# Kernel tuning notes

Measured on AMD Instinct MI355X. Metric: run time of the kernel, lower is better.

The kernel has to match this reference:

```python
import jax, jax.numpy as jnp
import numpy as np

T = 4096   # reference sequence length (concatenated virtual samples)
L = 4096   # modality sequence length
D_Q = 64   # reference feature dim
D_QK = 128 # projected query/key dim (before add_one -> 129)
D_V = 128  # value dim
N_IDS = 8  # number of virtual samples encoded in idx


def setup_inputs() -> dict:
    key = jax.random.key(0)
    ks = jax.random.split(key, 20)
    inp = {}
    inp['ref_data'] = jax.random.normal(ks[0], (1, 1, T, D_Q), jnp.float32)
    inp['ref_time'] = jnp.sort(jax.random.uniform(ks[1], (1, T), jnp.float32), axis=-1)
    inp['ref_idx'] = jnp.sort(jax.random.randint(ks[2], (T,), 0, N_IDS))
    inp['m1_data'] = jax.random.normal(ks[3], (1, 1, L, 130), jnp.float32)
    inp['m1_time'] = jnp.sort(jax.random.uniform(ks[4], (1, L), jnp.float32), axis=-1)
    inp['m1_idx'] = jnp.sort(jax.random.randint(ks[5], (L,), 0, N_IDS))
    inp['m2_data'] = jax.random.normal(ks[6], (1, 1, L, 66), jnp.float32)
    inp['m2_time'] = jnp.sort(jax.random.uniform(ks[7], (1, L), jnp.float32), axis=-1)
    inp['m2_idx'] = jnp.sort(jax.random.randint(ks[8], (L,), 0, N_IDS))
    s = 0.05
    inp['Wq'] = jax.random.normal(ks[9], (D_Q, D_QK), jnp.float32) * s
    inp['bq'] = jnp.zeros((D_QK,), jnp.float32)
    inp['Wk1'] = jax.random.normal(ks[10], (1, D_QK), jnp.float32) * s
    inp['bk1'] = jnp.zeros((D_QK,), jnp.float32)
    inp['Wv1'] = jax.random.normal(ks[11], (128, D_V), jnp.float32) * s
    inp['bv1'] = jnp.zeros((D_V,), jnp.float32)
    inp['Wk2'] = jax.random.normal(ks[12], (1, D_QK), jnp.float32) * s
    inp['bk2'] = jnp.zeros((D_QK,), jnp.float32)
    inp['Wv2'] = jax.random.normal(ks[13], (64, D_V), jnp.float32) * s
    inp['bv2'] = jnp.zeros((D_V,), jnp.float32)
    inp['log_tau1'] = jnp.zeros((), jnp.float32)  # log(init_tau=1)
    inp['log_tau2'] = jnp.zeros((), jnp.float32)
    return inp


def _add_one_q(x):  # add_one(x, dim=1): append ones on last axis
    return jnp.concatenate([x, jnp.ones(x.shape[:-1] + (1,), x.dtype)], axis=-1)


def _feat_k(x):  # add_one(x, dim=0): [ones, -x]
    return jnp.concatenate([jnp.ones(x.shape[:-1] + (1,), x.dtype), -x], axis=-1)


def _uni_attn(Q, mdata, q_t, kv_t, q_idx, kv_idx, Wk, bk, Wv, bv, log_tau):
    # qk_type='time': keys from last feature (timestamp), values from data[..., :-2]
    K = _feat_k(mdata[..., -1:] @ Wk + bk)          # (1,1,L,d_qk+1)
    V = mdata[..., :-2] @ Wv + bv                   # (1,1,L,d_v)
    tau = jnp.exp(log_tau)
    # gaussian weight: -(Q.K)^2 / tau
    A = -jnp.square(jnp.einsum('nhtc,nhlc->nhtl', Q, K)) / tau  # (1,1,T,L)
    causal = (q_t[:, :, None] >= kv_t[:, None, :]).astype(Q.dtype)[:, None]  # (1,1,T,L)
    neg_inf = jnp.array(-jnp.inf, Q.dtype)
    bm = jnp.where(q_idx[None, :, None] == kv_idx[None, None, :], jnp.zeros((), Q.dtype), neg_inf)  # (1,T,L)
    fully_masked = jnp.all(jnp.isneginf(bm), axis=-1, keepdims=True)
    safe = jnp.where(fully_masked, jnp.zeros((), Q.dtype), bm)[:, None]  # (1,1,T,L)
    A = jax.nn.softmax(A * causal + safe, axis=-1) * causal
    return jnp.einsum('nhtl,nhlc->nhtc', A, V)      # (1,1,T,d_v)


def reference(ref_data, ref_time, m1_data, m1_time, m2_data, m2_time,
              Wq, bq, Wk1, bk1, Wv1, bv1, Wk2, bk2, Wv2, bv2,
              log_tau1, log_tau2, ref_idx, m1_idx, m2_idx):
    Q = _add_one_q(ref_data @ Wq + bq)  # (1,1,T,d_qk+1)
    y1 = _uni_attn(Q, m1_data, ref_time, m1_time, ref_idx, m1_idx, Wk1, bk1, Wv1, bv1, log_tau1)
    y2 = _uni_attn(Q, m2_data, ref_time, m2_time, ref_idx, m2_idx, Wk2, bk2, Wv2, bv2, log_tau2)
    return jnp.concatenate([y1, y2], axis=-1)  # (1,1,T,2*d_v)
```

## Files before the change

kernel.cpp:

```cpp
#include <hip/hip_runtime.h>
#include <hip/hip_bf16.h>

#define TQ 4096
#define LK 4096
#define QT 16
#define NSPLIT 4
#define CHJ 32

template<bool BF> __device__ __forceinline__ float ld(const void* p, int i);
template<> __device__ __forceinline__ float ld<true>(const void* p, int i) {
    return __bfloat162float(((const __hip_bfloat16*)p)[i]);
}
template<> __device__ __forceinline__ float ld<false>(const void* p, int i) {
    return ((const float*)p)[i];
}
template<bool BF> __device__ __forceinline__ float2 ld2(const void* p, int i);
template<> __device__ __forceinline__ float2 ld2<false>(const void* p, int i) {
    return *(const float2*)((const float*)p + i);
}
template<> __device__ __forceinline__ float2 ld2<true>(const void* p, int i) {
    float2 r; r.x = ld<true>(p, i); r.y = ld<true>(p, i + 1); return r;
}
template<bool BF> __device__ __forceinline__ float4 ld4(const void* p, int i);
template<> __device__ __forceinline__ float4 ld4<false>(const void* p, int i) {
    return *(const float4*)((const float*)p + i);
}
template<> __device__ __forceinline__ float4 ld4<true>(const void* p, int i) {
    float4 r; r.x = ld<true>(p, i); r.y = ld<true>(p, i + 1);
    r.z = ld<true>(p, i + 2); r.w = ld<true>(p, i + 3); return r;
}
template<bool BF> __device__ __forceinline__ void st4(void* p, int i, float4 v);
template<> __device__ __forceinline__ void st4<true>(void* p, int i, float4 v) {
    __hip_bfloat16* o = (__hip_bfloat16*)p + i;
    o[0] = __float2bfloat16(v.x); o[1] = __float2bfloat16(v.y);
    o[2] = __float2bfloat16(v.z); o[3] = __float2bfloat16(v.w);
}
template<> __device__ __forceinline__ void st4<false>(void* p, int i, float4 v) {
    *(float4*)((float*)p + i) = v;
}

__device__ __forceinline__ bool sniff_bf16(const void* ref_time) {
    const int lane = threadIdx.x & 63;
    bool ok = true;
    if (lane < 32) {
        float v = __bfloat162float(((const __hip_bfloat16*)ref_time)[2 * lane]);
        ok = (v >= 0.0f) && (v <= 1.0f);
    }
    return __ballot(ok) == ~0ULL;
}

template<bool BF>
__device__ int ub_time(const void* arr, int n, float key) {
    int lo = 0, hi = n;
    while (lo < hi) { int mid = (lo + hi) >> 1; if (ld<BF>(arr, mid) <= key) lo = mid + 1; else hi = mid; }
    return lo;
}
__device__ int lb_int(const int* arr, int n, int key) {
    int lo = 0, hi = n;
    while (lo < hi) { int mid = (lo + hi) >> 1; if (arr[mid] < key) lo = mid + 1; else hi = mid; }
    return lo;
}
__device__ int ub_int(const int* arr, int n, int key) {
    int lo = 0, hi = n;
    while (lo < hi) { int mid = (lo + hi) >> 1; if (arr[mid] <= key) lo = mid + 1; else hi = mid; }
    return lo;
}

template<bool BF>
__device__ void prep_body(
    const void* ref_data, const void* ref_time, const int* ref_idx,
    const void* m1_time, const int* m1_idx, const void* m2_time, const int* m2_idx,
    const void* Wq, const void* bq,
    const void* Wk1, const void* bk1, const void* Wk2, const void* bk2,
    float* alpha1, float* beta1, float* alpha2, float* beta2,
    int* c1, int* s1, int* e1, int* c2, int* s2, int* e2)
{
    const int lane = threadIdx.x;
    const int t0 = blockIdx.x * 4;

    float rq[4];
    #pragma unroll
    for (int k = 0; k < 4; ++k) rq[k] = ld<BF>(ref_data, (t0 + k) * 64 + lane);

    const float bq0 = ld<BF>(bq, lane), bq1 = ld<BF>(bq, 64 + lane);
    float a0[4], a1[4];
    #pragma unroll
    for (int k = 0; k < 4; ++k) { a0[k] = bq0; a1[k] = bq1; }

    #pragma unroll 16
    for (int i = 0; i < 64; ++i) {
        const float w0 = ld<BF>(Wq, i * 128 + lane);
        const float w1 = ld<BF>(Wq, i * 128 + 64 + lane);
        #pragma unroll
        for (int k = 0; k < 4; ++k) {
            const float x = __shfl(rq[k], i);
            a0[k] = fmaf(x, w0, a0[k]);
            a1[k] = fmaf(x, w1, a1[k]);
        }
    }

    const float wk1lo = (lane >= 1) ? ld<BF>(Wk1, lane - 1) : 0.0f;
    const float wk1hi = ld<BF>(Wk1, lane + 63);
    const float bk1lo = (lane >= 1) ? ld<BF>(bk1, lane - 1) : 0.0f;
    const float bk1hi = ld<BF>(bk1, lane + 63);
    const float wk2lo = (lane >= 1) ? ld<BF>(Wk2, lane - 1) : 0.0f;
    const float wk2hi = ld<BF>(Wk2, lane + 63);
    const float bk2lo = (lane >= 1) ? ld<BF>(bk2, lane - 1) : 0.0f;
    const float bk2hi = ld<BF>(bk2, lane + 63);
    const float wk1sp = ld<BF>(Wk1, 127), bk1sp = ld<BF>(bk1, 127);
    const float wk2sp = ld<BF>(Wk2, 127), bk2sp = ld<BF>(bk2, 127);
    const float sp = (lane == 0) ? 1.0f : 0.0f;

    float red[16];
    #pragma unroll
    for (int k = 0; k < 4; ++k) {
        red[k * 4 + 0] = fmaf(a0[k], wk1lo, fmaf(a1[k], wk1hi, sp * wk1sp));
        red[k * 4 + 1] = sp * (a0[k] - bk1sp) - a0[k] * bk1lo - a1[k] * bk1hi;
        red[k * 4 + 2] = fmaf(a0[k], wk2lo, fmaf(a1[k], wk2hi, sp * wk2sp));
        red[k * 4 + 3] = sp * (a0[k] - bk2sp) - a0[k] * bk2lo - a1[k] * bk2hi;
    }
    #pragma unroll
    for (int o = 32; o >= 1; o >>= 1) {
        #pragma unroll
        for (int r = 0; r < 16; ++r) red[r] += __shfl_xor(red[r], o);
    }
    if (lane < 4) {
        const int t = t0 + lane;
        beta1[t]  = red[lane * 4 + 0];
        alpha1[t] = red[lane * 4 + 1];
        beta2[t]  = red[lane * 4 + 2];
        alpha2[t] = red[lane * 4 + 3];
    }

    if (lane < 24) {
        const int kind = lane >> 2, k = lane & 3, t = t0 + k;
        switch (kind) {
            case 0: c1[t] = ub_time<BF>(m1_time, LK, ld<BF>(ref_time, t)); break;
            case 1: c2[t] = ub_time<BF>(m2_time, LK, ld<BF>(ref_time, t)); break;
            case 2: s1[t] = lb_int(m1_idx, LK, ref_idx[t]); break;
            case 3: e1[t] = ub_int(m1_idx, LK, ref_idx[t]); break;
            case 4: s2[t] = lb_int(m2_idx, LK, ref_idx[t]); break;
            case 5: e2[t] = ub_int(m2_idx, LK, ref_idx[t]); break;
        }
    }
}

__global__ __launch_bounds__(64) void prep_kernel(
    const void* ref_data, const void* ref_time, const int* ref_idx,
    const void* m1_time, const int* m1_idx, const void* m2_time, const int* m2_idx,
    const void* Wq, const void* bq,
    const void* Wk1, const void* bk1, const void* Wk2, const void* bk2,
    float* alpha1, float* beta1, float* alpha2, float* beta2,
    int* c1, int* s1, int* e1, int* c2, int* s2, int* e2)
{
    if (sniff_bf16(ref_time))
        prep_body<true>(ref_data, ref_time, ref_idx, m1_time, m1_idx, m2_time, m2_idx,
                        Wq, bq, Wk1, bk1, Wk2, bk2,
                        alpha1, beta1, alpha2, beta2, c1, s1, e1, c2, s2, e2);
    else
        prep_body<false>(ref_data, ref_time, ref_idx, m1_time, m1_idx, m2_time, m2_idx,
                         Wq, bq, Wk1, bk1, Wk2, bk2,
                         alpha1, beta1, alpha2, beta2, c1, s1, e1, c2, s2, e2);
}

template<bool BF, int K, int DM>
__device__ void vproj_wave(const void* md, const void* Wv, const void* bv,
                           float* V, float* X, int rows0)
{
    const int lane = threadIdx.x & 63;
    const int cT = lane & 31;
    const int rG = lane >> 5;
    const int r0 = rows0 + rG * 4;
    const int c4 = cT * 4;

    const float4 bb = ld4<BF>(bv, c4);
    float4 acc[4] = {bb, bb, bb, bb};

    #pragma unroll 2
    for (int k = 0; k < K; k += 4) {
        const float4 w0 = ld4<BF>(Wv, (k + 0) * 128 + c4);
        const float4 w1 = ld4<BF>(Wv, (k + 1) * 128 + c4);
        const float4 w2 = ld4<BF>(Wv, (k + 2) * 128 + c4);
        const float4 w3 = ld4<BF>(Wv, (k + 3) * 128 + c4);
        float2 alo[4], ahi[4];
        #pragma unroll
        for (int r = 0; r < 4; ++r) {
            alo[r] = ld2<BF>(md, (r0 + r) * DM + k);
            ahi[r] = ld2<BF>(md, (r0 + r) * DM + k + 2);
        }
        #pragma unroll
        for (int r = 0; r < 4; ++r) {
            acc[r].x = fmaf(alo[r].x, w0.x, fmaf(alo[r].y, w1.x, fmaf(ahi[r].x, w2.x, fmaf(ahi[r].y, w3.x, acc[r].x))));
            acc[r].y = fmaf(alo[r].x, w0.y, fmaf(alo[r].y, w1.y, fmaf(ahi[r].x, w2.y, fmaf(ahi[r].y, w3.y, acc[r].y))));
            acc[r].z = fmaf(alo[r].x, w0.z, fmaf(alo[r].y, w1.z, fmaf(ahi[r].x, w2.z, fmaf(ahi[r].y, w3.z, acc[r].z))));
            acc[r].w = fmaf(alo[r].x, w0.w, fmaf(alo[r].y, w1.w, fmaf(ahi[r].x, w2.w, fmaf(ahi[r].y, w3.w, acc[r].w))));
        }
    }
    #pragma unroll
    for (int r = 0; r < 4; ++r)
        *(float4*)&V[(size_t)(r0 + r) * 128 + c4] = acc[r];
    if (rG == 0 && cT < 8)
        X[rows0 + cT] = ld<BF>(md, (rows0 + cT) * DM + DM - 1);
}

__global__ __launch_bounds__(64) void vproj_kernel(
    const void* __restrict__ ref_time,
    const void* m1_data, const void* Wv1, const void* bv1,
    const void* m2_data, const void* Wv2, const void* bv2,
    float* V1, float* V2, float* X1, float* X2)
{
    const int rows0 = blockIdx.x * 8;
    const int mod = blockIdx.y;
    const bool bf = sniff_bf16(ref_time);
    if (mod == 0) {
        if (bf) vproj_wave<true, 128, 130>(m1_data, Wv1, bv1, V1, X1, rows0);
        else    vproj_wave<false, 128, 130>(m1_data, Wv1, bv1, V1, X1, rows0);
    } else {
        if (bf) vproj_wave<true, 64, 66>(m2_data, Wv2, bv2, V2, X2, rows0);
        else    vproj_wave<false, 64, 66>(m2_data, Wv2, bv2, V2, X2, rows0);
    }
}

__global__ __launch_bounds__(128) void attn_kernel(
    const void* __restrict__ ref_time,
    const float* __restrict__ alpha1, const float* __restrict__ beta1,
    const float* __restrict__ alpha2, const float* __restrict__ beta2,
    const int* __restrict__ c1, const int* __restrict__ s1, const int* __restrict__ e1,
    const int* __restrict__ c2, const int* __restrict__ s2, const int* __restrict__ e2,
    const float* __restrict__ V1, const float* __restrict__ V2,
    const float* __restrict__ X1, const float* __restrict__ X2,
    const void* log_tau1, const void* log_tau2,
    float* __restrict__ Opart, float* __restrict__ Zpart)
{
    __shared__ float sW[2][CHJ * QT];
    __shared__ float sO[QT * 128];
    __shared__ float sZm[QT];

    const int tid = threadIdx.x;
    const int wid = tid >> 6, lane = tid & 63;
    const int t0 = blockIdx.x * QT, zb = blockIdx.y, mod = blockIdx.z;

    const bool bf = sniff_bf16(ref_time);
    const float* alpha = mod ? alpha2 : alpha1;
    const float* beta  = mod ? beta2  : beta1;
    const int* cA = mod ? c2 : c1;
    const int* sA = mod ? s2 : s1;
    const int* eA = mod ? e2 : e1;
    const float* V = mod ? V2 : V1;
    const float* X = mod ? X2 : X1;
    const void* ltp = mod ? log_tau2 : log_tau1;
    const float scale = __expf(-(bf ? ld<true>(ltp, 0) : ld<false>(ltp, 0)));

    const int q = lane & 15;
    const int t = t0 + q;
    int s = sA[t], e = eA[t];
    const int c = cA[t];
    if (s == e) { s = 0; e = LK; }
    const int cm = min(c, e);
    const float al = alpha[t], be = beta[t];

    int es = (cm > s) ? s : 0x7fffffff;
    int ec = (cm > s) ? cm : 0;
    #pragma unroll
    for (int o = 1; o < 64; o <<= 1) {
        es = min(es, __shfl_xor(es, o));
        ec = max(ec, __shfl_xor(ec, o));
    }
    int jlo = es, jhi = ec;
    if (jlo > jhi) { jlo = 0; jhi = 0; }
    const int W = jhi - jlo;
    const int chunk = (W + NSPLIT * 2 - 1) / (NSPLIT * 2);
    const int sub = zb * 2 + wid;
    const int lo = jlo + sub * chunk;
    int hi = min(jhi, lo + chunk); if (hi < lo) hi = lo;
    const int nch = (chunk + CHJ - 1) / CHJ;

    const int cT = lane & 31, qG = lane >> 5;
    const int jj = lane >> 4;
    float4 acc[8] = {{0,0,0,0},{0,0,0,0},{0,0,0,0},{0,0,0,0},
                     {0,0,0,0},{0,0,0,0},{0,0,0,0},{0,0,0,0}};
    float zacc = 0.0f;
    float* myW = sW[wid];
    const float4* __restrict__ Vg = (const float4*)V;

    for (int ci = 0; ci < nch; ++ci) {
        const int base = lo + ci * CHJ;
        const int jm = min(CHJ, hi - base);
        if (jm > 0) {
            #pragma unroll
            for (int p = 0; p < 8; ++p) {
                const int jr = jj + p * 4;
                const int j = base + jr;
                const bool ok = (jr < jm) && (j >= s) && (j < cm);
                const float x = X[min(j, LK - 1)];
                const float qk = fmaf(-be, x, al);
                const float w = ok ? __expf(-(qk * qk) * scale) : 0.0f;
                myW[jr * QT + q] = w;
                zacc += w;
            }
        }
        __syncthreads();
        if (jm > 0) {
            #pragma unroll 4
            for (int j = 0; j < jm; ++j) {
                const float4 v = Vg[(base + j) * 32 + cT];
                const float4* wv = (const float4*)&myW[j * QT + qG * 8];
                const float4 wA = wv[0], wB = wv[1];
                acc[0].x = fmaf(wA.x, v.x, acc[0].x); acc[0].y = fmaf(wA.x, v.y, acc[0].y);
                acc[0].z = fmaf(wA.x, v.z, acc[0].z); acc[0].w = fmaf(wA.x, v.w, acc[0].w);
                acc[1].x = fmaf(wA.y, v.x, acc[1].x); acc[1].y = fmaf(wA.y, v.y, acc[1].y);
                acc[1].z = fmaf(wA.y, v.z, acc[1].z); acc[1].w = fmaf(wA.y, v.w, acc[1].w);
                acc[2].x = fmaf(wA.z, v.x, acc[2].x); acc[2].y = fmaf(wA.z, v.y, acc[2].y);
                acc[2].z = fmaf(wA.z, v.z, acc[2].z); acc[2].w = fmaf(wA.z, v.w, acc[2].w);
                acc[3].x = fmaf(wA.w, v.x, acc[3].x); acc[3].y = fmaf(wA.w, v.y, acc[3].y);
                acc[3].z = fmaf(wA.w, v.z, acc[3].z); acc[3].w = fmaf(wA.w, v.w, acc[3].w);
                acc[4].x = fmaf(wB.x, v.x, acc[4].x); acc[4].y = fmaf(wB.x, v.y, acc[4].y);
                acc[4].z = fmaf(wB.x, v.z, acc[4].z); acc[4].w = fmaf(wB.x, v.w, acc[4].w);
                acc[5].x = fmaf(wB.y, v.x, acc[5].x); acc[5].y = fmaf(wB.y, v.y, acc[5].y);
                acc[5].z = fmaf(wB.y, v.z, acc[5].z); acc[5].w = fmaf(wB.y, v.w, acc[5].w);
                acc[6].x = fmaf(wB.z, v.x, acc[6].x); acc[6].y = fmaf(wB.z, v.y, acc[6].y);
                acc[6].z = fmaf(wB.z, v.z, acc[6].z); acc[6].w = fmaf(wB.z, v.w, acc[6].w);
                acc[7].x = fmaf(wB.w, v.x, acc[7].x); acc[7].y = fmaf(wB.w, v.y, acc[7].y);
                acc[7].z = fmaf(wB.w, v.z, acc[7].z); acc[7].w = fmaf(wB.w, v.w, acc[7].w);
            }
        }
        __syncthreads();
    }

    float z = zacc;
    z += __shfl_xor(z, 16);
    z += __shfl_xor(z, 32);

    const int part = zb * 2 + mod;
    if (wid == 0) {
        #pragma unroll
        for (int r = 0; r < 8; ++r)
            *(float4*)&sO[(qG * 8 + r) * 128 + cT * 4] = acc[r];
        if (lane < 16) sZm[lane] = z;
    }
    __syncthreads();
    if (wid == 1) {
        float4* Og = (float4*)Opart;
        #pragma unroll
        for (int r = 0; r < 8; ++r) {
            const float4 o0 = *(const float4*)&sO[(qG * 8 + r) * 128 + cT * 4];
            float4 o = acc[r];
            o.x += o0.x; o.y += o0.y; o.z += o0.z; o.w += o0.w;
            Og[((size_t)(part << 12) + (t0 + qG * 8 + r)) * 32 + cT] = o;
        }
        if (lane < 16) Zpart[(part << 12) + t0 + lane] = z + sZm[lane];
    }
}

__global__ __launch_bounds__(256) void finish_kernel(
    const void* __restrict__ ref_time,
    const int* __restrict__ c1, const int* __restrict__ s1, const int* __restrict__ e1,
    const int* __restrict__ c2, const int* __restrict__ s2, const int* __restrict__ e2,
    const float* __restrict__ Zpart, const float* __restrict__ Opart,
    void* __restrict__ out)
{
    const bool bf = sniff_bf16(ref_time);
    const int idx = blockIdx.x * 256 + threadIdx.x;
    const int t = idx >> 6;
    const int rem = idx & 63;
    const int mod = rem >> 5;
    const int c4 = rem & 31;

    const int* cA = mod ? c2 : c1;
    const int* sA = mod ? s2 : s1;
    const int* eA = mod ? e2 : e1;
    int s = sA[t], e = eA[t];
    const int c = cA[t];
    if (s == e) { s = 0; e = LK; }
    const int nnc = (e > c) ? (e - max(s, c)) : 0;

    float Z = (float)nnc;
    float4 o = {0, 0, 0, 0};
    const float4* Og = (const float4*)Opart;
    #pragma unroll
    for (int zb = 0; zb < NSPLIT; ++zb) {
        const int part = zb * 2 + mod;
        Z += Zpart[(part << 12) + t];
        const float4 p = Og[((size_t)(part << 12) + t) * 32 + c4];
        o.x += p.x; o.y += p.y; o.z += p.z; o.w += p.w;
    }
    const float inv = 1.0f / fmaxf(Z, 1.0e-20f);
    o.x *= inv; o.y *= inv; o.z *= inv; o.w *= inv;
    if (bf) st4<true>(out, t * 256 + mod * 128 + c4 * 4, o);
    else    st4<false>(out, t * 256 + mod * 128 + c4 * 4, o);
}

extern "C" void kernel_launch(void* const* d_in, const int* in_sizes, int n_in,
                              void* d_out, int out_size, void* d_ws, size_t ws_size,
                              hipStream_t stream)
{
    const void* ref_data = d_in[0];
    const void* ref_time = d_in[1];
    const int*  ref_idx  = (const int*)d_in[2];
    const void* m1_data  = d_in[3];
    const void* m1_time  = d_in[4];
    const int*  m1_idx   = (const int*)d_in[5];
    const void* m2_data  = d_in[6];
    const void* m2_time  = d_in[7];
    const int*  m2_idx   = (const int*)d_in[8];
    const void* Wq  = d_in[9];
    const void* bq  = d_in[10];
    const void* Wk1 = d_in[11];
    const void* bk1 = d_in[12];
    const void* Wv1 = d_in[13];
    const void* bv1 = d_in[14];
    const void* Wk2 = d_in[15];
    const void* bk2 = d_in[16];
    const void* Wv2 = d_in[17];
    const void* bv2 = d_in[18];
    const void* log_tau1 = d_in[19];
    const void* log_tau2 = d_in[20];

    float* ws = (float*)d_ws;
    float* alpha1 = ws + 0 * TQ;
    float* beta1  = ws + 1 * TQ;
    float* alpha2 = ws + 2 * TQ;
    float* beta2  = ws + 3 * TQ;
    int*   c1 = (int*)(ws + 4 * TQ);
    int*   c2 = (int*)(ws + 5 * TQ);
    int*   s1 = (int*)(ws + 6 * TQ);
    int*   e1 = (int*)(ws + 7 * TQ);
    int*   s2 = (int*)(ws + 8 * TQ);
    int*   e2 = (int*)(ws + 9 * TQ);
    float* X1 = ws + 10 * TQ;
    float* X2 = ws + 11 * TQ;
    float* V1 = ws + 12 * TQ;
    float* V2 = V1 + (size_t)LK * 128;
    float* Zpart = V2 + (size_t)LK * 128;
    float* Opart = Zpart + 8 * TQ;

    prep_kernel<<<dim3(TQ / 4), dim3(64), 0, stream>>>(
        ref_data, ref_time, ref_idx, m1_time, m1_idx, m2_time, m2_idx,
        Wq, bq, Wk1, bk1, Wk2, bk2,
        alpha1, beta1, alpha2, beta2, c1, s1, e1, c2, s2, e2);

    vproj_kernel<<<dim3(LK / 8, 2), dim3(64), 0, stream>>>(
        ref_time, m1_data, Wv1, bv1, m2_data, Wv2, bv2, V1, V2, X1, X2);

    attn_kernel<<<dim3(TQ / QT, NSPLIT, 2), dim3(128), 0, stream>>>(
        ref_time, alpha1, beta1, alpha2, beta2, c1, s1, e1, c2, s2, e2,
        V1, V2, X1, X2, log_tau1, log_tau2, Opart, Zpart);

    finish_kernel<<<dim3(TQ * 2 * 32 / 256), dim3(256), 0, stream>>>(
        ref_time, c1, s1, e1, c2, s2, e2, Zpart, Opart, (void*)d_out);
}
```

Baseline: 186.9 us.

## Fold key weights into Wq so prep computes four dot products per query

```diff
diff --git a/kernel.cpp b/kernel.cpp
--- a/kernel.cpp
+++ b/kernel.cpp
@@ -6,6 +6,8 @@
 #define QT 16
 #define NSPLIT 4
 #define CHJ 32
+#define PB 32
+#define PQ (TQ / PB)
 
 template<bool BF> __device__ __forceinline__ float ld(const void* p, int i);
 template<> __device__ __forceinline__ float ld<true>(const void* p, int i) {
@@ -49,12 +51,6 @@
     return __ballot(ok) == ~0ULL;
 }
 
-template<bool BF>
-__device__ int ub_time(const void* arr, int n, float key) {
-    int lo = 0, hi = n;
-    while (lo < hi) { int mid = (lo + hi) >> 1; if (ld<BF>(arr, mid) <= key) lo = mid + 1; else hi = mid; }
-    return lo;
-}
 __device__ int lb_int(const int* arr, int n, int key) {
     int lo = 0, hi = n;
     while (lo < hi) { int mid = (lo + hi) >> 1; if (arr[mid] < key) lo = mid + 1; else hi = mid; }
@@ -75,77 +71,81 @@
     float* alpha1, float* beta1, float* alpha2, float* beta2,
     int* c1, int* s1, int* e1, int* c2, int* s2, int* e2)
 {
-    const int lane = threadIdx.x;
-    const int t0 = blockIdx.x * 4;
-
-    float rq[4];
-    #pragma unroll
-    for (int k = 0; k < 4; ++k) rq[k] = ld<BF>(ref_data, (t0 + k) * 64 + lane);
-
-    const float bq0 = ld<BF>(bq, lane), bq1 = ld<BF>(bq, 64 + lane);
-    float a0[4], a1[4];
-    #pragma unroll
-    for (int k = 0; k < 4; ++k) { a0[k] = bq0; a1[k] = bq1; }
-
-    #pragma unroll 16
-    for (int i = 0; i < 64; ++i) {
-        const float w0 = ld<BF>(Wq, i * 128 + lane);
-        const float w1 = ld<BF>(Wq, i * 128 + 64 + lane);
-        #pragma unroll
-        for (int k = 0; k < 4; ++k) {
-            const float x = __shfl(rq[k], i);
-            a0[k] = fmaf(x, w0, a0[k]);
-            a1[k] = fmaf(x, w1, a1[k]);
-        }
-    }
-
-    const float wk1lo = (lane >= 1) ? ld<BF>(Wk1, lane - 1) : 0.0f;
-    const float wk1hi = ld<BF>(Wk1, lane + 63);
-    const float bk1lo = (lane >= 1) ? ld<BF>(bk1, lane - 1) : 0.0f;
-    const float bk1hi = ld<BF>(bk1, lane + 63);
-    const float wk2lo = (lane >= 1) ? ld<BF>(Wk2, lane - 1) : 0.0f;
-    const float wk2hi = ld<BF>(Wk2, lane + 63);
-    const float bk2lo = (lane >= 1) ? ld<BF>(bk2, lane - 1) : 0.0f;
-    const float bk2hi = ld<BF>(bk2, lane + 63);
-    const float wk1sp = ld<BF>(Wk1, 127), bk1sp = ld<BF>(bk1, 127);
-    const float wk2sp = ld<BF>(Wk2, 127), bk2sp = ld<BF>(bk2, 127);
-    const float sp = (lane == 0) ? 1.0f : 0.0f;
-
-    float red[16];
-    #pragma unroll
-    for (int k = 0; k < 4; ++k) {
-        red[k * 4 + 0] = fmaf(a0[k], wk1lo, fmaf(a1[k], wk1hi, sp * wk1sp));
-        red[k * 4 + 1] = sp * (a0[k] - bk1sp) - a0[k] * bk1lo - a1[k] * bk1hi;
-        red[k * 4 + 2] = fmaf(a0[k], wk2lo, fmaf(a1[k], wk2hi, sp * wk2sp));
-        red[k * 4 + 3] = sp * (a0[k] - bk2sp) - a0[k] * bk2lo - a1[k] * bk2hi;
-    }
-    #pragma unroll
-    for (int o = 32; o >= 1; o >>= 1) {
-        #pragma unroll
-        for (int r = 0; r < 16; ++r) red[r] += __shfl_xor(red[r], o);
-    }
-    if (lane < 4) {
-        const int t = t0 + lane;
-        beta1[t]  = red[lane * 4 + 0];
-        alpha1[t] = red[lane * 4 + 1];
-        beta2[t]  = red[lane * 4 + 2];
-        alpha2[t] = red[lane * 4 + 3];
-    }
-
-    if (lane < 24) {
-        const int kind = lane >> 2, k = lane & 3, t = t0 + k;
-        switch (kind) {
-            case 0: c1[t] = ub_time<BF>(m1_time, LK, ld<BF>(ref_time, t)); break;
-            case 1: c2[t] = ub_time<BF>(m2_time, LK, ld<BF>(ref_time, t)); break;
-            case 2: s1[t] = lb_int(m1_idx, LK, ref_idx[t]); break;
-            case 3: e1[t] = ub_int(m1_idx, LK, ref_idx[t]); break;
-            case 4: s2[t] = lb_int(m2_idx, LK, ref_idx[t]); break;
-            case 5: e2[t] = ub_int(m2_idx, LK, ref_idx[t]); break;
-        }
-    }
-}
-
-__global__ __launch_bounds__(64) void prep_kernel(
+    __shared__ float ut[64][4];
+    __shared__ float cst[4];
+    __shared__ int tabs[4][8];
+
+    const int tid = threadIdx.x;
+    const int i = tid >> 2, r = tid & 3;
+
+    {
+        const void* w = (r == 0) ? Wk1 : (r == 1) ? bk1 : (r == 2) ? Wk2 : bk2;
+        const bool isA = (r & 1);
+        float acc = isA ? ld<BF>(Wq, i * 128) : 0.0f;
+        const float sgn = isA ? -1.0f : 1.0f;
+        #pragma unroll 4
+        for (int d = 1; d < 128; ++d)
+            acc = fmaf(sgn * ld<BF>(Wq, i * 128 + d), ld<BF>(w, d - 1), acc);
+        ut[i][r] = acc;
+    }
+    if (tid < 4) {
+        const void* w = (tid == 0) ? Wk1 : (tid == 1) ? bk1 : (tid == 2) ? Wk2 : bk2;
+        const bool isA = (tid & 1);
+        float c = isA ? ld<BF>(bq, 0) : 0.0f;
+        const float sgn = isA ? -1.0f : 1.0f;
+        #pragma unroll 4
+        for (int d = 1; d < 128; ++d)
+            c = fmaf(sgn * ld<BF>(bq, d), ld<BF>(w, d - 1), c);
+        c += sgn * ld<BF>(w, 127);
+        cst[tid] = c;
+    }
+    if (tid >= 4 && tid < 36) {
+        const int k = tid - 4;
+        const int sid = k & 7, rest = k >> 3;
+        const int modk = rest & 1, kind = rest >> 1;
+        const int* arr = modk ? m2_idx : m1_idx;
+        tabs[modk * 2 + kind][sid] = kind ? ub_int(arr, LK, sid) : lb_int(arr, LK, sid);
+    }
+    __syncthreads();
+
+    const int q = tid & 127;
+    const int t = blockIdx.x * PQ + q;
+    if (tid < 128) {
+        float4 acc = {cst[0], cst[1], cst[2], cst[3]};
+        #pragma unroll
+        for (int ii = 0; ii < 64; ii += 4) {
+            const float4 rv = ld4<BF>(ref_data, t * 64 + ii);
+            const float4 u0 = *(const float4*)ut[ii + 0];
+            const float4 u1 = *(const float4*)ut[ii + 1];
+            const float4 u2 = *(const float4*)ut[ii + 2];
+            const float4 u3 = *(const float4*)ut[ii + 3];
+            acc.x = fmaf(rv.x, u0.x, fmaf(rv.y, u1.x, fmaf(rv.z, u2.x, fmaf(rv.w, u3.x, acc.x))));
+            acc.y = fmaf(rv.x, u0.y, fmaf(rv.y, u1.y, fmaf(rv.z, u2.y, fmaf(rv.w, u3.y, acc.y))));
+            acc.z = fmaf(rv.x, u0.z, fmaf(rv.y, u1.z, fmaf(rv.z, u2.z, fmaf(rv.w, u3.z, acc.z))));
+            acc.w = fmaf(rv.x, u0.w, fmaf(rv.y, u1.w, fmaf(rv.z, u2.w, fmaf(rv.w, u3.w, acc.w))));
+        }
+        beta1[t] = acc.x; alpha1[t] = acc.y;
+        beta2[t] = acc.z; alpha2[t] = acc.w;
+    } else {
+        const float qt = ld<BF>(ref_time, t);
+        const int g = ref_idx[t];
+        int lo1 = 0, hi1 = LK, lo2 = 0, hi2 = LK;
+        #pragma unroll
+        for (int it = 0; it < 13; ++it) {
+            const int mA = min((lo1 + hi1) >> 1, LK - 1);
+            const int mB = min((lo2 + hi2) >> 1, LK - 1);
+            const float v1 = ld<BF>(m1_time, mA);
+            const float v2 = ld<BF>(m2_time, mB);
+            if (lo1 < hi1) { if (v1 <= qt) lo1 = mA + 1; else hi1 = mA; }
+            if (lo2 < hi2) { if (v2 <= qt) lo2 = mB + 1; else hi2 = mB; }
+        }
+        c1[t] = lo1; c2[t] = lo2;
+        s1[t] = tabs[0][g]; e1[t] = tabs[1][g];
+        s2[t] = tabs[2][g]; e2[t] = tabs[3][g];
+    }
+}
+
+__global__ __launch_bounds__(256) void prep_kernel(
     const void* ref_data, const void* ref_time, const int* ref_idx,
     const void* m1_time, const int* m1_idx, const void* m2_time, const int* m2_idx,
     const void* Wq, const void* bq,
@@ -434,7 +434,7 @@
     float* Zpart = V2 + (size_t)LK * 128;
     float* Opart = Zpart + 8 * TQ;
 
-    prep_kernel<<<dim3(TQ / 4), dim3(64), 0, stream>>>(
+    prep_kernel<<<dim3(PB), dim3(256), 0, stream>>>(
         ref_data, ref_time, ref_idx, m1_time, m1_idx, m2_time, m2_idx,
         Wq, bq, Wk1, bk1, Wk2, bk2,
         alpha1, beta1, alpha2, beta2, c1, s1, e1, c2, s2, e2);
```

New measurement: 179.3 us. 4.0% less time.
